# Optimization experiments

Hardware: AMD Instinct MI355X
Metric: run time of the kernel (lower is better)

## Reference

```python
import jax, jax.numpy as jnp
import numpy as np
import math

N_PATCH = 32768
DIM = 512
L_TOK = 64
W_SIZE = 64
STRIDE = 32


def setup_inputs() -> dict:
    key = jax.random.key(0)
    ks = jax.random.split(key, 12)
    d = DIM
    inp = {
        'feats': jax.random.normal(ks[0], (N_PATCH, d), dtype=jnp.float32),
        'coords': jax.random.uniform(ks[1], (N_PATCH, 2), dtype=jnp.float32),
        'mask': jnp.zeros((N_PATCH,), dtype=bool),
        'z': jax.random.normal(ks[2], (L_TOK, d), dtype=jnp.float32),
        'Wq': jax.random.normal(ks[3], (d, d), dtype=jnp.float32) / math.sqrt(d),
        'Wk': jax.random.normal(ks[4], (d, d), dtype=jnp.float32) / math.sqrt(d),
        'Wv': jax.random.normal(ks[5], (d, d), dtype=jnp.float32) / math.sqrt(d),
        'w1': jax.random.normal(ks[6], (d, 2), dtype=jnp.float32) / math.sqrt(2.0),
        'b1': jnp.zeros((d,), dtype=jnp.float32),
        'w2': jax.random.normal(ks[7], (d, d), dtype=jnp.float32) / math.sqrt(d),
        'b2': jnp.zeros((d,), dtype=jnp.float32),
        'Wo': jax.random.normal(ks[8], (d, d), dtype=jnp.float32) / math.sqrt(d),
        'bo': jnp.zeros((d,), dtype=jnp.float32),
    }
    return inp


def _lstcwa(feats, coords, z, Wq, Wk, Wv, w1, b1, w2, b2, Wo, bo):
    # mask is all-False -> feats kept as-is; N divisible by L -> equal segments
    N, D = feats.shape
    L = z.shape[0]
    n = N // L                       # patches per segment
    nwin = -(-n // STRIDE)           # windows per segment (ceil)

    # window offsets within a segment, [nwin, w]; last window truncated via mask
    off = jnp.arange(nwin)[:, None] * STRIDE + jnp.arange(W_SIZE)[None, :]
    valid = off < n                  # [nwin, w]
    idx = jnp.arange(L)[:, None, None] * n + jnp.minimum(off, n - 1)[None]  # [L,nwin,w]

    q = z @ Wq.T                     # [L, D]
    kf = feats @ Wk.T                # [N, D]
    vf = feats @ Wv.T

    k_win = kf[idx]                  # [L, nwin, w, D]
    v_win = vf[idx]
    c_win = coords[idx]              # [L, nwin, w, 2]

    vf32 = valid.astype(feats.dtype)                      # [nwin, w]
    cnt = vf32.sum(-1)                                    # [nwin]
    c_mean = jnp.einsum('lnwc,nw->lnc', c_win, vf32) / cnt[None, :, None]
    delta = (c_win - c_mean[:, :, None, :]) * vf32[None, :, :, None]

    pos = jax.nn.relu(delta @ w1.T + b1) @ w2.T + b2      # [L, nwin, w, D]
    k_win = k_win + pos

    logits = jnp.einsum('ld,lnwd->lnw', q, k_win) / math.sqrt(D)
    logits = jnp.where(valid[None], logits, -1e9)
    attn = jax.nn.softmax(logits, axis=-1)                # [L, nwin, w]

    z_win = jnp.einsum('lnw,lnwd->lnd', attn, v_win)      # [L, nwin, D]
    # return_alpha=False path: z_l_acc / max(1, len(attn_acc)=0) -> SUM over windows
    Z = z_win.sum(1)                                      # [L, D]
    return Z @ Wo.T + bo


def reference(feats, coords, mask, z, Wq, Wk, Wv, w1, b1, w2, b2, Wo, bo):
    # mask is all-False by construction (static shapes under jit)
    return _lstcwa(feats, coords, z, Wq, Wk, Wv, w1, b1, w2, b2, Wo, bo)
```

## Files before the change

### kernel.cpp

```cpp
#include <hip/hip_runtime.h>
#include <math.h>

#define DIMV 512
#define LTOK 64
#define SEG  512
#define NWIN 16
#define WSZ  64
#define INV_SQRT_D 0.044194173824159216f

__device__ __forceinline__ float wave_sum(float v) {
#pragma unroll
  for (int m = 1; m < 64; m <<= 1) v += __shfl_xor(v, m, 64);
  return v;
}

__global__ __launch_bounds__(256, 4) void k_q(const float* __restrict__ z,
    const float* __restrict__ Wq, const float* __restrict__ coords,
    float* __restrict__ q, float* __restrict__ cmean)
{
  int l = blockIdx.x >> 4, c = blockIdx.x & 15;
  int wave = threadIdx.x >> 6, lane = threadIdx.x & 63;
  int e0 = lane << 3;
  const float* zp = z + l * DIMV + e0;
  float x0[8];
  *(float4*)&x0[0] = *(const float4*)zp;
  *(float4*)&x0[4] = *(const float4*)(zp + 4);
  int d0 = c * 32 + wave * 8;
  float rf[8][8];
#pragma unroll
  for (int k = 0; k < 8; ++k) {
    const float* rp = Wq + (size_t)(d0 + k) * DIMV + e0;
    *(float4*)&rf[k][0] = *(const float4*)rp;
    *(float4*)&rf[k][4] = *(const float4*)(rp + 4);
  }
#pragma unroll
  for (int k = 0; k < 8; ++k) {
    float p = 0.f;
#pragma unroll
    for (int j = 0; j < 8; ++j) p = fmaf(rf[k][j], x0[j], p);
    p = wave_sum(p);
    if (lane == k) q[l * DIMV + d0 + k] = p;
  }
  if (wave == 0) {
    int n = c;
    int nvalid = (n == 15) ? 32 : 64;
    bool v = lane < nvalid;
    float cx = 0.f, cy = 0.f;
    if (v) {
      const float* cp = coords + ((size_t)(l * SEG + n * 32 + lane)) * 2;
      cx = cp[0]; cy = cp[1];
    }
    float inv = 1.0f / (float)nvalid;
    float mx = wave_sum(cx) * inv;
    float my = wave_sum(cy) * inv;
    if (lane == 0) {
      cmean[(l * NWIN + n) * 2]     = mx;
      cmean[(l * NWIN + n) * 2 + 1] = my;
    }
  }
}

__global__ __launch_bounds__(256) void k_qproj(const float* __restrict__ q,
    const float* __restrict__ Wk, const float* __restrict__ w2,
    const float* __restrict__ b2, float* __restrict__ qk,
    float* __restrict__ qw2, float* __restrict__ qb2)
{
  int l = blockIdx.x >> 3, ec = blockIdx.x & 7;
  int wave = threadIdx.x >> 6, lane = threadIdx.x & 63;
  int t = threadIdx.x;
  __shared__ float qs[DIMV];
  __shared__ float pk[4][64], pw[4][64];
  qs[t] = q[l * DIMV + t];
  qs[t + 256] = q[l * DIMV + t + 256];
  __syncthreads();
  int e = ec * 64 + lane;
  int d0 = wave * 128;
  float ak = 0.f, aw = 0.f;
#pragma unroll 8
  for (int dd = 0; dd < 128; ++dd) {
    int d = d0 + dd;
    float qd = qs[d];
    ak = fmaf(qd, Wk[(size_t)d * DIMV + e], ak);
    aw = fmaf(qd, w2[(size_t)d * DIMV + e], aw);
  }
  pk[wave][lane] = ak;
  pw[wave][lane] = aw;
  __syncthreads();
  if (wave == 0) {
    qk[l * DIMV + e] = pk[0][lane] + pk[1][lane] + pk[2][lane] + pk[3][lane];
  } else if (wave == 1) {
    qw2[l * DIMV + e] = pw[0][lane] + pw[1][lane] + pw[2][lane] + pw[3][lane];
  } else if (wave == 2 && ec == 0) {
    int e0 = lane << 3;
    float pb = 0.f;
#pragma unroll
    for (int j = 0; j < 8; ++j) pb = fmaf(qs[e0 + j], b2[e0 + j], pb);
    pb = wave_sum(pb);
    if (lane == 0) qb2[l] = pb;
  }
}

__global__ __launch_bounds__(256, 4) void k_pos(
    const float* __restrict__ coords, const float* __restrict__ cmean,
    const float* __restrict__ qw2,   const float* __restrict__ qb2,
    const float* __restrict__ w1,    const float* __restrict__ b1,
    float* __restrict__ pos)
{
  int widx = blockIdx.x;
  int l = widx >> 4, n = widx & 15;
  int t = threadIdx.x;
  int p = t & 63, qd = t >> 6;
  __shared__ float w1s[2 * DIMV], b1s[DIMV], qws[DIMV], part[4][WSZ];
#pragma unroll
  for (int i = 0; i < 4; ++i) w1s[t + 256 * i] = w1[t + 256 * i];
#pragma unroll
  for (int i = 0; i < 2; ++i) {
    b1s[t + 256 * i] = b1[t + 256 * i];
    qws[t + 256 * i] = qw2[l * DIMV + t + 256 * i];
  }
  __syncthreads();
  int nvalid = (n == 15) ? 32 : 64;
  int off = n * 32 + p;
  int row = (p < nvalid) ? off : (SEG - 1);
  float dx = coords[((size_t)(l * SEG + row)) * 2]     - cmean[(l * NWIN + n) * 2];
  float dy = coords[((size_t)(l * SEG + row)) * 2 + 1] - cmean[(l * NWIN + n) * 2 + 1];
  float acc = 0.f;
  int d0 = qd * 128;
#pragma unroll 4
  for (int dd = 0; dd < 128; ++dd) {
    int d = d0 + dd;
    float h = fmaf(dx, w1s[2 * d], fmaf(dy, w1s[2 * d + 1], b1s[d]));
    acc = fmaf(fmaxf(h, 0.f), qws[d], acc);
  }
  part[qd][p] = acc;
  __syncthreads();
  if (t < 64) {
    pos[(size_t)widx * WSZ + p] =
        part[0][p] + part[1][p] + part[2][p] + part[3][p] + qb2[l];
  }
}

__global__ __launch_bounds__(256, 4) void k_stream(
    const float* __restrict__ feats, const float* __restrict__ qk,
    const float* __restrict__ pos,   float* __restrict__ numA,
    float* __restrict__ numB, float* __restrict__ denA, float* __restrict__ denB)
{
  int l = blockIdx.x >> 4, c = blockIdx.x & 15;
  int wave = threadIdx.x >> 6, lane = threadIdx.x & 63;
  int e0 = lane << 3, t = threadIdx.x;

  float qk8[8];
  {
    const float* p = qk + l * DIMV + e0;
    *(float4*)&qk8[0] = *(const float4*)p;
    *(float4*)&qk8[4] = *(const float4*)(p + 4);
  }
  const float* posA = pos + ((size_t)(l * NWIN) + c) * WSZ;
  const float* posB = pos + ((size_t)(l * NWIN) + (c > 0 ? c - 1 : 0)) * WSZ + 32;

  float aA[8], aB[8];
#pragma unroll
  for (int j = 0; j < 8; ++j) { aA[j] = 0.f; aB[j] = 0.f; }
  float dA = 0.f, dB = 0.f;

  int rbase = c * 32 + wave * 8;
  const float* fbase = feats + ((size_t)(l * SEG + rbase)) * DIMV;
#pragma unroll
  for (int k = 0; k < 8; ++k) {
    int rl = wave * 8 + k;
    float f8[8];
    const float* rp = fbase + (size_t)k * DIMV + e0;
    *(float4*)&f8[0] = *(const float4*)rp;
    *(float4*)&f8[4] = *(const float4*)(rp + 4);
    float dot = 0.f;
#pragma unroll
    for (int j = 0; j < 8; ++j) dot = fmaf(qk8[j], f8[j], dot);
    dot = wave_sum(dot);
    float eh = __expf((dot + posA[rl]) * INV_SQRT_D);
    float el = 0.f;
    if (c > 0) el = __expf((dot + posB[rl]) * INV_SQRT_D);
    dA += eh; dB += el;
#pragma unroll
    for (int j = 0; j < 8; ++j) {
      aA[j] = fmaf(eh, f8[j], aA[j]);
      aB[j] = fmaf(el, f8[j], aB[j]);
    }
  }

  __shared__ float sA[4][DIMV], sB[4][DIMV];
  __shared__ float sd[4][2];
  *(float4*)&sA[wave][e0]     = *(float4*)&aA[0];
  *(float4*)&sA[wave][e0 + 4] = *(float4*)&aA[4];
  *(float4*)&sB[wave][e0]     = *(float4*)&aB[0];
  *(float4*)&sB[wave][e0 + 4] = *(float4*)&aB[4];
  if (lane == 0) { sd[wave][0] = dA; sd[wave][1] = dB; }
  __syncthreads();
  size_t ob = ((size_t)(l * NWIN) + c) * DIMV;
#pragma unroll
  for (int i = 0; i < 2; ++i) {
    int e = t + 256 * i;
    numA[ob + e] = sA[0][e] + sA[1][e] + sA[2][e] + sA[3][e];
    numB[ob + e] = sB[0][e] + sB[1][e] + sB[2][e] + sB[3][e];
  }
  if (t == 0) {
    denA[l * NWIN + c] = sd[0][0] + sd[1][0] + sd[2][0] + sd[3][0];
    denB[l * NWIN + c] = sd[0][1] + sd[1][1] + sd[2][1] + sd[3][1];
  }
}

__global__ __launch_bounds__(512) void k_ured(
    const float* __restrict__ numA, const float* __restrict__ numB,
    const float* __restrict__ denA, const float* __restrict__ denB,
    float* __restrict__ U)
{
  int l = blockIdx.x, t = threadIdx.x;
  __shared__ float dinv[NWIN];
  if (t < NWIN) {
    float d = denA[l * NWIN + t];
    if (t < NWIN - 1) d += denB[l * NWIN + t + 1];
    dinv[t] = 1.0f / d;
  }
  __syncthreads();
  float u = 0.f;
#pragma unroll
  for (int n = 0; n < NWIN; ++n) {
    float na = numA[((size_t)(l * NWIN) + n) * DIMV + t];
    if (n < NWIN - 1) na += numB[((size_t)(l * NWIN) + n + 1) * DIMV + t];
    u = fmaf(na, dinv[n], u);
  }
  U[l * DIMV + t] = u;
}

__global__ __launch_bounds__(256, 4) void k_uv(const float* __restrict__ U,
    const float* __restrict__ Wv, float* __restrict__ tbuf)
{
  int l = blockIdx.x >> 4, c = blockIdx.x & 15;
  int wave = threadIdx.x >> 6, lane = threadIdx.x & 63;
  int e0 = lane << 3;
  const float* up = U + l * DIMV + e0;
  float x0[8];
  *(float4*)&x0[0] = *(const float4*)up;
  *(float4*)&x0[4] = *(const float4*)(up + 4);
  int f0 = c * 32 + wave * 8;
  float rf[8][8];
#pragma unroll
  for (int k = 0; k < 8; ++k) {
    const float* rp = Wv + (size_t)(f0 + k) * DIMV + e0;
    *(float4*)&rf[k][0] = *(const float4*)rp;
    *(float4*)&rf[k][4] = *(const float4*)(rp + 4);
  }
#pragma unroll
  for (int k = 0; k < 8; ++k) {
    float p = 0.f;
#pragma unroll
    for (int j = 0; j < 8; ++j) p = fmaf(rf[k][j], x0[j], p);
    p = wave_sum(p);
    if (lane == k) tbuf[l * DIMV + f0 + k] = p;
  }
}

__global__ __launch_bounds__(256, 4) void k_out(const float* __restrict__ tbuf,
    const float* __restrict__ Wo, const float* __restrict__ bo,
    float* __restrict__ out)
{
  int l = blockIdx.x >> 4, c = blockIdx.x & 15;
  int wave = threadIdx.x >> 6, lane = threadIdx.x & 63;
  int e0 = lane << 3;
  const float* tp = tbuf + l * DIMV + e0;
  float x0[8];
  *(float4*)&x0[0] = *(const float4*)tp;
  *(float4*)&x0[4] = *(const float4*)(tp + 4);
  int d0 = c * 32 + wave * 8;
  float rf[8][8];
#pragma unroll
  for (int k = 0; k < 8; ++k) {
    const float* rp = Wo + (size_t)(d0 + k) * DIMV + e0;
    *(float4*)&rf[k][0] = *(const float4*)rp;
    *(float4*)&rf[k][4] = *(const float4*)(rp + 4);
  }
#pragma unroll
  for (int k = 0; k < 8; ++k) {
    float p = 0.f;
#pragma unroll
    for (int j = 0; j < 8; ++j) p = fmaf(rf[k][j], x0[j], p);
    p = wave_sum(p);
    if (lane == k) out[l * DIMV + d0 + k] = p + bo[d0 + k];
  }
}

extern "C" void kernel_launch(void* const* d_in, const int* in_sizes, int n_in,
                              void* d_out, int out_size, void* d_ws, size_t ws_size,
                              hipStream_t stream) {
  (void)in_sizes; (void)n_in; (void)out_size; (void)ws_size;
  const float* feats  = (const float*)d_in[0];
  const float* coords = (const float*)d_in[1];
  const float* z   = (const float*)d_in[3];
  const float* Wq  = (const float*)d_in[4];
  const float* Wk  = (const float*)d_in[5];
  const float* Wv  = (const float*)d_in[6];
  const float* w1  = (const float*)d_in[7];
  const float* b1  = (const float*)d_in[8];
  const float* w2  = (const float*)d_in[9];
  const float* b2  = (const float*)d_in[10];
  const float* Wo  = (const float*)d_in[11];
  const float* bo  = (const float*)d_in[12];
  float* out = (float*)d_out;

  float* q     = (float*)d_ws;
  float* qk    = q     + LTOK * DIMV;
  float* qw2   = qk    + LTOK * DIMV;
  float* qb2   = qw2   + LTOK * DIMV;
  float* cmean = qb2   + LTOK;
  float* pos   = cmean + LTOK * NWIN * 2;
  float* numA  = pos   + LTOK * NWIN * WSZ;
  float* numB  = numA  + LTOK * NWIN * DIMV;
  float* denA  = numB  + LTOK * NWIN * DIMV;
  float* denB  = denA  + LTOK * NWIN;
  float* U     = denB  + LTOK * NWIN;
  float* tbuf  = U     + LTOK * DIMV;

  hipLaunchKernelGGL(k_q,      dim3(LTOK * NWIN), dim3(256), 0, stream,
                     z, Wq, coords, q, cmean);
  hipLaunchKernelGGL(k_qproj,  dim3(LTOK * 8),    dim3(256), 0, stream,
                     q, Wk, w2, b2, qk, qw2, qb2);
  hipLaunchKernelGGL(k_pos,    dim3(LTOK * NWIN), dim3(256), 0, stream,
                     coords, cmean, qw2, qb2, w1, b1, pos);
  hipLaunchKernelGGL(k_stream, dim3(LTOK * NWIN), dim3(256), 0, stream,
                     feats, qk, pos, numA, numB, denA, denB);
  hipLaunchKernelGGL(k_ured,   dim3(LTOK),        dim3(512), 0, stream,
                     numA, numB, denA, denB, U);
  hipLaunchKernelGGL(k_uv,     dim3(LTOK * NWIN), dim3(256), 0, stream,
                     U, Wv, tbuf);
  hipLaunchKernelGGL(k_out,    dim3(LTOK * NWIN), dim3(256), 0, stream,
                     tbuf, Wo, bo, out);
}
```

Before: 58.79 us.

## Fuse window reduction into Wv projection and restructure stream kernel loads

```diff
diff --git a/kernel.cpp b/kernel.cpp
--- a/kernel.cpp
+++ b/kernel.cpp
@@ -145,54 +145,58 @@
     const float* __restrict__ pos,   float* __restrict__ numA,
     float* __restrict__ numB, float* __restrict__ denA, float* __restrict__ denB)
 {
-  int l = blockIdx.x >> 4, c = blockIdx.x & 15;
-  int wave = threadIdx.x >> 6, lane = threadIdx.x & 63;
-  int e0 = lane << 3, t = threadIdx.x;
-
-  float qk8[8];
-  {
-    const float* p = qk + l * DIMV + e0;
-    *(float4*)&qk8[0] = *(const float4*)p;
-    *(float4*)&qk8[4] = *(const float4*)(p + 4);
-  }
+  int bid = blockIdx.x;
+  int swz = (bid & 7) * 128 + (bid >> 3);
+  int l = swz >> 4, c = swz & 15;
+  int wave = threadIdx.x >> 6, lane = threadIdx.x & 63;
+  int col = lane << 2;
+  int t = threadIdx.x;
+
+  float4 qka = *(const float4*)(qk + l * DIMV + col);
+  float4 qkb = *(const float4*)(qk + l * DIMV + 256 + col);
   const float* posA = pos + ((size_t)(l * NWIN) + c) * WSZ;
   const float* posB = pos + ((size_t)(l * NWIN) + (c > 0 ? c - 1 : 0)) * WSZ + 32;
 
+  int rbase = c * 32 + wave * 8;
+  const float* fbase = feats + ((size_t)(l * SEG + rbase)) * DIMV;
+
+  float4 fa[8], fb[8];
+#pragma unroll
+  for (int k = 0; k < 8; ++k) {
+    fa[k] = *(const float4*)(fbase + (size_t)k * DIMV + col);
+    fb[k] = *(const float4*)(fbase + (size_t)k * DIMV + 256 + col);
+  }
+
   float aA[8], aB[8];
 #pragma unroll
   for (int j = 0; j < 8; ++j) { aA[j] = 0.f; aB[j] = 0.f; }
   float dA = 0.f, dB = 0.f;
 
-  int rbase = c * 32 + wave * 8;
-  const float* fbase = feats + ((size_t)(l * SEG + rbase)) * DIMV;
 #pragma unroll
   for (int k = 0; k < 8; ++k) {
     int rl = wave * 8 + k;
-    float f8[8];
-    const float* rp = fbase + (size_t)k * DIMV + e0;
-    *(float4*)&f8[0] = *(const float4*)rp;
-    *(float4*)&f8[4] = *(const float4*)(rp + 4);
-    float dot = 0.f;
-#pragma unroll
-    for (int j = 0; j < 8; ++j) dot = fmaf(qk8[j], f8[j], dot);
+    float dot = fa[k].x * qka.x + fa[k].y * qka.y + fa[k].z * qka.z + fa[k].w * qka.w
+              + fb[k].x * qkb.x + fb[k].y * qkb.y + fb[k].z * qkb.z + fb[k].w * qkb.w;
     dot = wave_sum(dot);
     float eh = __expf((dot + posA[rl]) * INV_SQRT_D);
-    float el = 0.f;
-    if (c > 0) el = __expf((dot + posB[rl]) * INV_SQRT_D);
+    float el = (c > 0) ? __expf((dot + posB[rl]) * INV_SQRT_D) : 0.f;
     dA += eh; dB += el;
-#pragma unroll
-    for (int j = 0; j < 8; ++j) {
-      aA[j] = fmaf(eh, f8[j], aA[j]);
-      aB[j] = fmaf(el, f8[j], aB[j]);
-    }
+    aA[0] = fmaf(eh, fa[k].x, aA[0]); aA[1] = fmaf(eh, fa[k].y, aA[1]);
+    aA[2] = fmaf(eh, fa[k].z, aA[2]); aA[3] = fmaf(eh, fa[k].w, aA[3]);
+    aA[4] = fmaf(eh, fb[k].x, aA[4]); aA[5] = fmaf(eh, fb[k].y, aA[5]);
+    aA[6] = fmaf(eh, fb[k].z, aA[6]); aA[7] = fmaf(eh, fb[k].w, aA[7]);
+    aB[0] = fmaf(el, fa[k].x, aB[0]); aB[1] = fmaf(el, fa[k].y, aB[1]);
+    aB[2] = fmaf(el, fa[k].z, aB[2]); aB[3] = fmaf(el, fa[k].w, aB[3]);
+    aB[4] = fmaf(el, fb[k].x, aB[4]); aB[5] = fmaf(el, fb[k].y, aB[5]);
+    aB[6] = fmaf(el, fb[k].z, aB[6]); aB[7] = fmaf(el, fb[k].w, aB[7]);
   }
 
   __shared__ float sA[4][DIMV], sB[4][DIMV];
   __shared__ float sd[4][2];
-  *(float4*)&sA[wave][e0]     = *(float4*)&aA[0];
-  *(float4*)&sA[wave][e0 + 4] = *(float4*)&aA[4];
-  *(float4*)&sB[wave][e0]     = *(float4*)&aB[0];
-  *(float4*)&sB[wave][e0 + 4] = *(float4*)&aB[4];
+  *(float4*)&sA[wave][col]       = *(float4*)&aA[0];
+  *(float4*)&sA[wave][256 + col] = *(float4*)&aA[4];
+  *(float4*)&sB[wave][col]       = *(float4*)&aB[0];
+  *(float4*)&sB[wave][256 + col] = *(float4*)&aB[4];
   if (lane == 0) { sd[wave][0] = dA; sd[wave][1] = dB; }
   __syncthreads();
   size_t ob = ((size_t)(l * NWIN) + c) * DIMV;
@@ -208,12 +212,17 @@
   }
 }
 
-__global__ __launch_bounds__(512) void k_ured(
+__global__ __launch_bounds__(256, 4) void k_uv(
     const float* __restrict__ numA, const float* __restrict__ numB,
     const float* __restrict__ denA, const float* __restrict__ denB,
-    float* __restrict__ U)
-{
-  int l = blockIdx.x, t = threadIdx.x;
+    const float* __restrict__ Wv,  float* __restrict__ tbuf)
+{
+  int bid = blockIdx.x;
+  int swz = (bid & 7) * 128 + (bid >> 3);
+  int l = swz >> 4, c = swz & 15;
+  int wave = threadIdx.x >> 6, lane = threadIdx.x & 63;
+  int e0 = lane << 3, t = threadIdx.x;
+  __shared__ float us[DIMV];
   __shared__ float dinv[NWIN];
   if (t < NWIN) {
     float d = denA[l * NWIN + t];
@@ -221,26 +230,22 @@
     dinv[t] = 1.0f / d;
   }
   __syncthreads();
-  float u = 0.f;
-#pragma unroll
-  for (int n = 0; n < NWIN; ++n) {
-    float na = numA[((size_t)(l * NWIN) + n) * DIMV + t];
-    if (n < NWIN - 1) na += numB[((size_t)(l * NWIN) + n + 1) * DIMV + t];
-    u = fmaf(na, dinv[n], u);
-  }
-  U[l * DIMV + t] = u;
-}
-
-__global__ __launch_bounds__(256, 4) void k_uv(const float* __restrict__ U,
-    const float* __restrict__ Wv, float* __restrict__ tbuf)
-{
-  int l = blockIdx.x >> 4, c = blockIdx.x & 15;
-  int wave = threadIdx.x >> 6, lane = threadIdx.x & 63;
-  int e0 = lane << 3;
-  const float* up = U + l * DIMV + e0;
+#pragma unroll
+  for (int i = 0; i < 2; ++i) {
+    int e = t + 256 * i;
+    float u = 0.f;
+#pragma unroll
+    for (int n = 0; n < NWIN; ++n) {
+      float na = numA[((size_t)(l * NWIN) + n) * DIMV + e];
+      if (n < NWIN - 1) na += numB[((size_t)(l * NWIN) + n + 1) * DIMV + e];
+      u = fmaf(na, dinv[n], u);
+    }
+    us[e] = u;
+  }
+  __syncthreads();
   float x0[8];
-  *(float4*)&x0[0] = *(const float4*)up;
-  *(float4*)&x0[4] = *(const float4*)(up + 4);
+  *(float4*)&x0[0] = *(float4*)&us[e0];
+  *(float4*)&x0[4] = *(float4*)&us[e0 + 4];
   int f0 = c * 32 + wave * 8;
   float rf[8][8];
 #pragma unroll
@@ -316,8 +321,7 @@
   float* numB  = numA  + LTOK * NWIN * DIMV;
   float* denA  = numB  + LTOK * NWIN * DIMV;
   float* denB  = denA  + LTOK * NWIN;
-  float* U     = denB  + LTOK * NWIN;
-  float* tbuf  = U     + LTOK * DIMV;
+  float* tbuf  = denB  + LTOK * NWIN;
 
   hipLaunchKernelGGL(k_q,      dim3(LTOK * NWIN), dim3(256), 0, stream,
                      z, Wq, coords, q, cmean);
@@ -327,10 +331,8 @@
                      coords, cmean, qw2, qb2, w1, b1, pos);
   hipLaunchKernelGGL(k_stream, dim3(LTOK * NWIN), dim3(256), 0, stream,
                      feats, qk, pos, numA, numB, denA, denB);
-  hipLaunchKernelGGL(k_ured,   dim3(LTOK),        dim3(512), 0, stream,
-                     numA, numB, denA, denB, U);
   hipLaunchKernelGGL(k_uv,     dim3(LTOK * NWIN), dim3(256), 0, stream,
-                     U, Wv, tbuf);
+                     numA, numB, denA, denB, Wv, tbuf);
   hipLaunchKernelGGL(k_out,    dim3(LTOK * NWIN), dim3(256), 0, stream,
                      tbuf, Wo, bo, out);
 }
```

After: 59.18 us. Within noise of the previous version (+0.7%).
